# Kernel tuning notes

Measured on AMD Instinct MI355X. Metric: run time of the kernel, lower is better.

The kernel has to match this reference:

```python
import jax, jax.numpy as jnp
import numpy as np

B, S, D, H = 2, 2048, 1024, 16
HD = D // H  # head_dim = 64


def setup_inputs() -> dict:
    key = jax.random.key(0)
    ks = jax.random.split(key, 12)
    scale = 1.0 / np.sqrt(D)
    inp = {
        "query": jax.random.normal(ks[0], (B, S, D), jnp.float32),
        "key": jax.random.normal(ks[1], (B, S, D), jnp.float32),
        "value": jax.random.normal(ks[2], (B, S, D), jnp.float32),
        # causal mask, True = masked out; shape [B, q_len, k_len]
        "mask": jnp.broadcast_to(
            jnp.triu(jnp.ones((S, S), jnp.bool_), k=1), (B, S, S)
        ),
        "Wq": jax.random.normal(ks[3], (D, D), jnp.float32) * scale,
        "bq": jnp.zeros((D,), jnp.float32),
        "Wk": jax.random.normal(ks[4], (D, D), jnp.float32) * scale,
        "bk": jnp.zeros((D,), jnp.float32),
        "Wv": jax.random.normal(ks[5], (D, D), jnp.float32) * scale,
        "bv": jnp.zeros((D,), jnp.float32),
        "Wo": jax.random.normal(ks[6], (D, D), jnp.float32) * scale,
        "bo": jnp.zeros((D,), jnp.float32),
    }
    return inp


def _split_heads(x):
    b, s, _ = x.shape
    return x.reshape(b, s, H, HD).transpose(0, 2, 1, 3)  # [B,H,S,HD]


def reference(query, key, value, mask, Wq, bq, Wk, bk, Wv, bv, Wo, bo):
    # Linear layers use torch convention: y = x @ W.T + b, W is [out, in]
    q = _split_heads(query @ Wq.T + bq)
    k = _split_heads(key @ Wk.T + bk)
    v = _split_heads(value @ Wv.T + bv)
    scores = jnp.einsum("bhqd,bhkd->bhqk", q, k) / jnp.sqrt(jnp.float32(HD))
    # normalized mask [B,1,q,k]; True means masked
    scores = jnp.where(mask[:, None, :, :], jnp.finfo(scores.dtype).min, scores)
    attn = jax.nn.softmax(scores, axis=-1)  # dropout is identity in eval
    ctx = jnp.einsum("bhqk,bhkd->bhqd", attn, v)
    merged = ctx.transpose(0, 2, 1, 3).reshape(query.shape[0], -1, D)
    out = merged @ Wo.T + bo
    return out
```

## Files before the change

### kernel.cpp

```cpp
#include <hip/hip_runtime.h>

#define B_ 2
#define S_ 2048
#define D_ 1024
#define H_ 16
#define HD_ 64
#define M_ (B_ * S_)

typedef __bf16 bf16x8 __attribute__((ext_vector_type(8)));
typedef float f32x4 __attribute__((ext_vector_type(4)));

__device__ inline unsigned short f2bf(float f) {
    unsigned int u = __builtin_bit_cast(unsigned int, f);
    u += 0x7fffu + ((u >> 16) & 1u);
    return (unsigned short)(u >> 16);
}

__device__ inline unsigned int cvt_pk_bf16(float lo, float hi) {
    unsigned int r;
    asm("v_cvt_pk_bf16_f32 %0, %1, %2" : "=v"(r) : "v"(lo), "v"(hi));
    return r;
}

__device__ inline float fexp2(float x) { return __builtin_amdgcn_exp2f(x); }

__device__ inline void barrier_fence() {
    asm volatile("" ::: "memory");
    __builtin_amdgcn_s_barrier();
    asm volatile("" ::: "memory");
}

__device__ inline void async_ld16(const unsigned short* g, unsigned short* l) {
    __builtin_amdgcn_global_load_lds(
        (const __attribute__((address_space(1))) unsigned int*)g,
        (__attribute__((address_space(3))) unsigned int*)l, 16, 0, 0);
}

__global__ __launch_bounds__(256) void cvt_all(
    const float* __restrict__ i0, const float* __restrict__ i1, const float* __restrict__ i2,
    const float* __restrict__ i3, const float* __restrict__ i4, const float* __restrict__ i5,
    const float* __restrict__ i6,
    unsigned short* __restrict__ o0, unsigned short* __restrict__ o1, unsigned short* __restrict__ o2,
    unsigned short* __restrict__ o3, unsigned short* __restrict__ o4, unsigned short* __restrict__ o5,
    unsigned short* __restrict__ o6, int nbig, int nsmall) {
    int z = blockIdx.y;
    const float* in = (z == 0) ? i0 : (z == 1) ? i1 : (z == 2) ? i2 : (z == 3) ? i3
                     : (z == 4) ? i4 : (z == 5) ? i5 : i6;
    unsigned short* out = (z == 0) ? o0 : (z == 1) ? o1 : (z == 2) ? o2 : (z == 3) ? o3
                         : (z == 4) ? o4 : (z == 5) ? o5 : o6;
    int n = (z < 3) ? nbig : nsmall;
    int i = (blockIdx.x * 256 + threadIdx.x) * 4;
    if (i >= n) return;
    float4 v = *(const float4*)(in + i);
    ushort4 o;
    o.x = f2bf(v.x); o.y = f2bf(v.y); o.z = f2bf(v.z); o.w = f2bf(v.w);
    *(ushort4*)(out + i) = o;
}

__device__ inline void gemm_compute(const unsigned short* __restrict__ A,
                                    const unsigned short* __restrict__ W,
                                    int K, int m0, int n0,
                                    unsigned short* As0, unsigned short* As1,
                                    unsigned short* Bs0, unsigned short* Bs1,
                                    f32x4 acc[4][4]) {
    const int t = threadIdx.x;
    const int lane = t & 63, wave = t >> 6;
    const int ml = lane & 15, quad = lane >> 4;
    const int wr = (wave >> 1) * 64, wc = (wave & 1) * 64;
    const int srow = lane >> 2;
    const int schunk = (lane & 3) ^ ((lane >> 4) & 3);

    const f32x4 zero = {0.f, 0.f, 0.f, 0.f};
    for (int i = 0; i < 4; i++)
        for (int j = 0; j < 4; j++) acc[i][j] = zero;

    const int niter = K >> 5;

    auto issue = [&](int kt, unsigned short* As, unsigned short* Bs) {
        int k0 = kt << 5;
        for (int i = 0; i < 2; i++) {
            int r = wave * 32 + i * 16;
            async_ld16(A + (size_t)(m0 + r + srow) * K + k0 + schunk * 8, As + r * 32);
            async_ld16(W + (size_t)(n0 + r + srow) * K + k0 + schunk * 8, Bs + r * 32);
        }
    };

    issue(0, As0, Bs0);
    issue(1, As1, Bs1);
    asm volatile("s_waitcnt vmcnt(4)" ::: "memory");
    barrier_fence();

    for (int kt = 0; kt < niter; kt++) {
        unsigned short* As = (kt & 1) ? As1 : As0;
        unsigned short* Bs = (kt & 1) ? Bs1 : Bs0;

        bf16x8 af[4], bfr[4];
        for (int i = 0; i < 4; i++)
            af[i] = *(const bf16x8*)(As + (wr + i * 16 + ml) * 32 + ((quad ^ (ml >> 2)) << 3));
        for (int j = 0; j < 4; j++)
            bfr[j] = *(const bf16x8*)(Bs + (wc + j * 16 + ml) * 32 + ((quad ^ (ml >> 2)) << 3));
        for (int i = 0; i < 4; i++)
            for (int j = 0; j < 4; j++)
                acc[i][j] = __builtin_amdgcn_mfma_f32_16x16x32_bf16(af[i], bfr[j], acc[i][j], 0, 0, 0);

        barrier_fence();
        if (kt + 2 < niter) {
            issue(kt + 2, As, Bs);
            asm volatile("s_waitcnt vmcnt(4)" ::: "memory");
        } else {
            asm volatile("s_waitcnt vmcnt(0)" ::: "memory");
        }
        barrier_fence();
    }
}

__global__ __launch_bounds__(256) void gemm_qkv(
    const unsigned short* __restrict__ xq, const unsigned short* __restrict__ xk,
    const unsigned short* __restrict__ xv,
    const unsigned short* __restrict__ wq, const unsigned short* __restrict__ wk,
    const unsigned short* __restrict__ wv,
    const float* __restrict__ bq, const float* __restrict__ bk, const float* __restrict__ bv,
    unsigned short* __restrict__ oq, unsigned short* __restrict__ ok,
    unsigned short* __restrict__ ov) {
    extern __shared__ __align__(16) unsigned short smem[];
    unsigned short* As0 = smem;
    unsigned short* As1 = smem + 4096;
    unsigned short* Bs0 = smem + 8192;
    unsigned short* Bs1 = smem + 12288;

    int f = blockIdx.x + (blockIdx.y << 3) + (blockIdx.z << 8);
    int l = (f & 7) * 96 + (f >> 3);
    int bx = l & 7, by = (l >> 3) & 31, z = l >> 8;

    const unsigned short *A, *W;
    const float* bias;
    unsigned short* out;
    if (z == 0) { A = xq; W = wq; bias = bq; out = oq; }
    else if (z == 1) { A = xk; W = wk; bias = bk; out = ok; }
    else { A = xv; W = wv; bias = bv; out = ov; }

    int m0 = by * 128, n0 = bx * 128;
    f32x4 acc[4][4];
    gemm_compute(A, W, D_, m0, n0, As0, As1, Bs0, Bs1, acc);

    const int t = threadIdx.x, lane = t & 63, wave = t >> 6;
    const int ml = lane & 15, quad = lane >> 4;
    const int wr = (wave >> 1) * 64, wc = (wave & 1) * 64;

    unsigned short* Cs = smem;
    const float sc = (z == 0) ? 0.1803368801111204f : 1.0f;
    for (int i = 0; i < 4; i++)
        for (int j = 0; j < 4; j++) {
            int col = wc + j * 16 + ml;
            float bb = bias[n0 + col];
            for (int rg = 0; rg < 4; rg++) {
                int row = wr + i * 16 + quad * 4 + rg;
                unsigned short v = f2bf((acc[i][j][rg] + bb) * sc);
                if (z < 2) Cs[row * 136 + col] = v;
                else       Cs[col * 136 + row] = v;
            }
        }
    __syncthreads();

    const int r = t >> 1, hf = t & 1;
    if (z < 2) {
        unsigned short* dst = out + (size_t)(m0 + r) * D_ + n0 + hf * 64;
        const unsigned short* src = Cs + r * 136 + hf * 64;
        for (int i = 0; i < 8; i++)
            *(uint4*)(dst + i * 8) = *(const uint4*)(src + i * 8);
    } else {
        int n = n0 + r, h = n >> 6, d = n & 63;
        int b = m0 >> 11, s0 = m0 & 2047;
        unsigned short* dst = ov + ((size_t)((b * H_ + h) * 64 + d)) * S_ + s0 + hf * 64;
        const unsigned short* src = Cs + r * 136 + hf * 64;
        for (int i = 0; i < 8; i++)
            *(uint4*)(dst + i * 8) = *(const uint4*)(src + i * 8);
    }
}

__global__ __launch_bounds__(256) void gemm_out(const unsigned short* __restrict__ A,
                                                const unsigned short* __restrict__ W,
                                                const float* __restrict__ bias,
                                                float* __restrict__ out) {
    __shared__ unsigned short As0[128 * 32], As1[128 * 32], Bs0[128 * 32], Bs1[128 * 32];

    int f = blockIdx.x + (blockIdx.y << 3);
    int l = (f & 7) * 32 + (f >> 3);
    int bx = l & 7, by = l >> 3;

    int m0 = by * 128, n0 = bx * 128;
    f32x4 acc[4][4];
    gemm_compute(A, W, D_, m0, n0, As0, As1, Bs0, Bs1, acc);

    const int t = threadIdx.x, lane = t & 63, wave = t >> 6;
    const int ml = lane & 15, quad = lane >> 4;
    const int wr = (wave >> 1) * 64, wc = (wave & 1) * 64;
    for (int i = 0; i < 4; i++)
        for (int j = 0; j < 4; j++) {
            int n = n0 + wc + j * 16 + ml;
            float bb = bias[n];
            for (int rg = 0; rg < 4; rg++) {
                int m = m0 + wr + i * 16 + quad * 4 + rg;
                out[(size_t)m * D_ + n] = acc[i][j][rg] + bb;
            }
        }
}

__global__ __launch_bounds__(256) void attn_kernel(const unsigned short* __restrict__ qm,
                                                   const unsigned short* __restrict__ km,
                                                   const unsigned short* __restrict__ vt,
                                                   unsigned short* __restrict__ ctx) {
    __shared__ unsigned short Ks[128 * 64];
    __shared__ unsigned short Vs[64 * 128];

    const int g = blockIdx.x >> 5;
    const int qb = (g & 1) ? (g >> 1) : (31 - (g >> 1));
    const int bh = blockIdx.x & 31;
    const int b = bh >> 4, h = bh & 15;
    const size_t vbase = (size_t)bh * S_ * 64;
    const int t = threadIdx.x, lane = t & 63, wave = t >> 6;
    const int ml = lane & 15, quad = lane >> 4;
    const int lrow = lane >> 3;
    const int gchunk = (lane & 7) ^ lrow;
    const int vrow = lane >> 4;
    const int q0 = qb * 64;

    bf16x8 qf[2];
    {
        int qrow = q0 + wave * 16 + ml;
        const unsigned short* qp = qm + (size_t)(b * S_ + qrow) * D_ + h * 64;
        qf[0] = *(const bf16x8*)(qp + quad * 8);
        qf[1] = *(const bf16x8*)(qp + 32 + quad * 8);
    }

    const f32x4 zero = {0.f, 0.f, 0.f, 0.f};
    f32x4 acc[4];
    for (int j = 0; j < 4; j++) acc[j] = zero;
    float m_i = -INFINITY, l_i = 0.f;

    const int ntiles = (qb + 2) >> 1;

    auto issue_K = [&](int kt) {
        for (int i = 0; i < 4; i++) {
            int r = wave * 32 + i * 8;
            async_ld16(km + (size_t)(b * S_ + kt * 128 + r + lrow) * D_ + h * 64 + gchunk * 8,
                       Ks + r * 64);
        }
    };
    auto issue_V = [&](int kt) {
        for (int i = 0; i < 4; i++) {
            int dd = wave * 16 + i * 4;
            int d = dd + vrow;
            async_ld16(vt + vbase + (size_t)d * S_ + kt * 128 + (((lane & 15) ^ (d & 15)) << 3),
                       Vs + dd * 128);
        }
    };

    issue_K(0);
    issue_V(0);
    asm volatile("s_waitcnt vmcnt(0)" ::: "memory");
    barrier_fence();

    for (int kt = 0; kt < ntiles; kt++) {
        f32x4 sacc[8];
        for (int n = 0; n < 8; n++) sacc[n] = zero;
        __builtin_amdgcn_s_setprio(1);
        for (int n = 0; n < 8; n++)
            for (int kk = 0; kk < 2; kk++) {
                bf16x8 kf = *(const bf16x8*)(Ks + (n * 16 + ml) * 64 +
                                             (((kk * 4 + quad) ^ (ml & 7)) << 3));
                sacc[n] = __builtin_amdgcn_mfma_f32_16x16x32_bf16(kf, qf[kk], sacc[n], 0, 0, 0);
            }
        __builtin_amdgcn_s_setprio(0);

        const bool last = (kt == ntiles - 1);
        const int qidx = q0 + wave * 16 + ml;
        if (last) {
            for (int n = 0; n < 8; n++)
                for (int rg = 0; rg < 4; rg++) {
                    int kidx = kt * 128 + n * 16 + quad * 4 + rg;
                    if (kidx > qidx) sacc[n][rg] = -3.0e38f;
                }
        }

        float m01 = fmaxf(fmaxf(sacc[0][0], sacc[0][1]), fmaxf(sacc[0][2], sacc[0][3]));
        float m1 = fmaxf(fmaxf(sacc[1][0], sacc[1][1]), fmaxf(sacc[1][2], sacc[1][3]));
        float m2 = fmaxf(fmaxf(sacc[2][0], sacc[2][1]), fmaxf(sacc[2][2], sacc[2][3]));
        float m3 = fmaxf(fmaxf(sacc[3][0], sacc[3][1]), fmaxf(sacc[3][2], sacc[3][3]));
        float m4 = fmaxf(fmaxf(sacc[4][0], sacc[4][1]), fmaxf(sacc[4][2], sacc[4][3]));
        float m5 = fmaxf(fmaxf(sacc[5][0], sacc[5][1]), fmaxf(sacc[5][2], sacc[5][3]));
        float m6 = fmaxf(fmaxf(sacc[6][0], sacc[6][1]), fmaxf(sacc[6][2], sacc[6][3]));
        float m7 = fmaxf(fmaxf(sacc[7][0], sacc[7][1]), fmaxf(sacc[7][2], sacc[7][3]));
        float mx = fmaxf(fmaxf(fmaxf(m01, m1), fmaxf(m2, m3)),
                         fmaxf(fmaxf(m4, m5), fmaxf(m6, m7)));
        mx = fmaxf(mx, __shfl_xor(mx, 16));
        mx = fmaxf(mx, __shfl_xor(mx, 32));
        if (!__all(mx <= m_i + 8.0f)) {
            float mc = fmaxf(m_i, mx);
            float al = fexp2(m_i - mc);
            m_i = mc;
            float alT[4];
            for (int rg = 0; rg < 4; rg++) alT[rg] = __shfl(al, quad * 4 + rg);
            for (int j = 0; j < 4; j++)
                for (int rg = 0; rg < 4; rg++) acc[j][rg] *= alT[rg];
            l_i *= al;
        }
        for (int n = 0; n < 8; n++)
            for (int rg = 0; rg < 4; rg++) sacc[n][rg] = fexp2(sacc[n][rg] - m_i);
        float s0 = (sacc[0][0] + sacc[0][1]) + (sacc[0][2] + sacc[0][3]);
        float s1 = (sacc[1][0] + sacc[1][1]) + (sacc[1][2] + sacc[1][3]);
        float s2 = (sacc[2][0] + sacc[2][1]) + (sacc[2][2] + sacc[2][3]);
        float s3 = (sacc[3][0] + sacc[3][1]) + (sacc[3][2] + sacc[3][3]);
        float s4 = (sacc[4][0] + sacc[4][1]) + (sacc[4][2] + sacc[4][3]);
        float s5 = (sacc[5][0] + sacc[5][1]) + (sacc[5][2] + sacc[5][3]);
        float s6 = (sacc[6][0] + sacc[6][1]) + (sacc[6][2] + sacc[6][3]);
        float s7 = (sacc[7][0] + sacc[7][1]) + (sacc[7][2] + sacc[7][3]);
        float rs = ((s0 + s1) + (s2 + s3)) + ((s4 + s5) + (s6 + s7));
        rs += __shfl_xor(rs, 16);
        rs += __shfl_xor(rs, 32);
        l_i += rs;

        asm volatile("s_waitcnt vmcnt(0)" ::: "memory");
        barrier_fence();
        if (kt + 1 < ntiles) issue_K(kt + 1);

        __builtin_amdgcn_s_setprio(1);
        for (int n2 = 0; n2 < 4; n2++) {
            union { bf16x8 v; unsigned int w[4]; } pk;
            pk.w[0] = cvt_pk_bf16(sacc[2 * n2][0], sacc[2 * n2][1]);
            pk.w[1] = cvt_pk_bf16(sacc[2 * n2][2], sacc[2 * n2][3]);
            pk.w[2] = cvt_pk_bf16(sacc[2 * n2 + 1][0], sacc[2 * n2 + 1][1]);
            pk.w[3] = cvt_pk_bf16(sacc[2 * n2 + 1][2], sacc[2 * n2 + 1][3]);
            const int c0 = 4 * n2 + (quad >> 1);
            const int qo = (quad & 1) << 2;
            for (int j = 0; j < 4; j++) {
                int row = j * 16 + ml;
                union { bf16x8 v; uint2 d2[2]; } vv;
                vv.d2[0] = *(const uint2*)(Vs + row * 128 + (((c0 ^ (row & 15)) << 3) + qo));
                vv.d2[1] = *(const uint2*)(Vs + row * 128 + ((((c0 + 2) ^ (row & 15)) << 3) + qo));
                acc[j] = __builtin_amdgcn_mfma_f32_16x16x32_bf16(pk.v, vv.v, acc[j], 0, 0, 0);
            }
        }
        __builtin_amdgcn_s_setprio(0);

        if (kt + 1 < ntiles) {
            asm volatile("s_waitcnt vmcnt(0)" ::: "memory");
            barrier_fence();
            issue_V(kt + 1);
        }
    }

    float inv[4];
    for (int rg = 0; rg < 4; rg++) inv[rg] = __builtin_amdgcn_rcpf(__shfl(l_i, quad * 4 + rg));
    for (int j = 0; j < 4; j++) {
        int d = j * 16 + ml;
        for (int rg = 0; rg < 4; rg++) {
            int srow = q0 + wave * 16 + quad * 4 + rg;
            ctx[((size_t)(b * S_ + srow)) * D_ + h * 64 + d] = f2bf(acc[j][rg] * inv[rg]);
        }
    }
}

extern "C" void kernel_launch(void* const* d_in, const int* in_sizes, int n_in,
                              void* d_out, int out_size, void* d_ws, size_t ws_size,
                              hipStream_t stream) {
    const float* query = (const float*)d_in[0];
    const float* key_ = (const float*)d_in[1];
    const float* value = (const float*)d_in[2];
    const float* Wq = (const float*)d_in[4];
    const float* bq = (const float*)d_in[5];
    const float* Wk = (const float*)d_in[6];
    const float* bk = (const float*)d_in[7];
    const float* Wv = (const float*)d_in[8];
    const float* bv = (const float*)d_in[9];
    const float* Wo = (const float*)d_in[10];
    const float* bo = (const float*)d_in[11];
    float* out = (float*)d_out;

    const size_t XE = (size_t)M_ * D_;
    const size_t WE = (size_t)D_ * D_;
    char* ws = (char*)d_ws;
    unsigned short* xq = (unsigned short*)ws; ws += XE * 2;
    unsigned short* xk = (unsigned short*)ws; ws += XE * 2;
    unsigned short* xv = (unsigned short*)ws; ws += XE * 2;
    unsigned short* wqb = (unsigned short*)ws; ws += WE * 2;
    unsigned short* wkb = (unsigned short*)ws; ws += WE * 2;
    unsigned short* wvb = (unsigned short*)ws; ws += WE * 2;
    unsigned short* wob = (unsigned short*)ws; ws += WE * 2;
    unsigned short* qmb = (unsigned short*)ws; ws += XE * 2;
    unsigned short* kmb = (unsigned short*)ws; ws += XE * 2;
    unsigned short* vt = (unsigned short*)ws; ws += XE * 2;
    unsigned short* ctx = (unsigned short*)ws; ws += XE * 2;

    cvt_all<<<dim3(XE / 1024, 7), 256, 0, stream>>>(
        query, key_, value, Wq, Wk, Wv, Wo,
        xq, xk, xv, wqb, wkb, wvb, wob, (int)XE, (int)WE);

    gemm_qkv<<<dim3(D_ / 128, M_ / 128, 3), 256, 34816, stream>>>(
        xq, xk, xv, wqb, wkb, wvb, bq, bk, bv, qmb, kmb, vt);

    attn_kernel<<<dim3(1024), 256, 0, stream>>>(qmb, kmb, vt, ctx);

    gemm_out<<<dim3(D_ / 128, M_ / 128), 256, 0, stream>>>(ctx, wob, bo, out);
}
```

Baseline: 240.1 us.

## Double-buffer K/V tiles and pair complementary query blocks per attention workgroup

The attention kernel now keeps two LDS buffers for K and V and prefetches the next tile while computing the current one, with one barrier per tile instead of two. Each workgroup processes two query blocks (qb and 31-qb) so every block does the same causal work, and the grid is halved to 512. The row-max and row-sum cross-lane reductions are deferred: the max shuffle runs only on the rescale path and the sum shuffle once per query block. LDS use doubles, which may lower occupancy, and the grid is half as large.

```diff
diff --git a/kernel.cpp b/kernel.cpp
--- a/kernel.cpp
+++ b/kernel.cpp
@@ -210,11 +210,10 @@
                                                    const unsigned short* __restrict__ km,
                                                    const unsigned short* __restrict__ vt,
                                                    unsigned short* __restrict__ ctx) {
-    __shared__ unsigned short Ks[128 * 64];
-    __shared__ unsigned short Vs[64 * 128];
-
-    const int g = blockIdx.x >> 5;
-    const int qb = (g & 1) ? (g >> 1) : (31 - (g >> 1));
+    __shared__ unsigned short Ks[2][128 * 64];
+    __shared__ unsigned short Vs[2][64 * 128];
+
+    const int p = blockIdx.x >> 5;
     const int bh = blockIdx.x & 31;
     const int b = bh >> 4, h = bh & 15;
     const size_t vbase = (size_t)bh * S_ * 64;
@@ -223,140 +222,144 @@
     const int lrow = lane >> 3;
     const int gchunk = (lane & 7) ^ lrow;
     const int vrow = lane >> 4;
-    const int q0 = qb * 64;
-
-    bf16x8 qf[2];
-    {
-        int qrow = q0 + wave * 16 + ml;
-        const unsigned short* qp = qm + (size_t)(b * S_ + qrow) * D_ + h * 64;
-        qf[0] = *(const bf16x8*)(qp + quad * 8);
-        qf[1] = *(const bf16x8*)(qp + 32 + quad * 8);
-    }
-
-    const f32x4 zero = {0.f, 0.f, 0.f, 0.f};
-    f32x4 acc[4];
-    for (int j = 0; j < 4; j++) acc[j] = zero;
-    float m_i = -INFINITY, l_i = 0.f;
-
-    const int ntiles = (qb + 2) >> 1;
-
-    auto issue_K = [&](int kt) {
+
+    auto issue_K = [&](int kt, int bb) {
         for (int i = 0; i < 4; i++) {
             int r = wave * 32 + i * 8;
             async_ld16(km + (size_t)(b * S_ + kt * 128 + r + lrow) * D_ + h * 64 + gchunk * 8,
-                       Ks + r * 64);
+                       Ks[bb] + r * 64);
         }
     };
-    auto issue_V = [&](int kt) {
+    auto issue_V = [&](int kt, int bb) {
         for (int i = 0; i < 4; i++) {
             int dd = wave * 16 + i * 4;
             int d = dd + vrow;
             async_ld16(vt + vbase + (size_t)d * S_ + kt * 128 + (((lane & 15) ^ (d & 15)) << 3),
-                       Vs + dd * 128);
+                       Vs[bb] + dd * 128);
         }
     };
 
-    issue_K(0);
-    issue_V(0);
+    const f32x4 zero = {0.f, 0.f, 0.f, 0.f};
+
+    issue_K(0, 0);
+    issue_V(0, 0);
     asm volatile("s_waitcnt vmcnt(0)" ::: "memory");
     barrier_fence();
 
-    for (int kt = 0; kt < ntiles; kt++) {
-        f32x4 sacc[8];
-        for (int n = 0; n < 8; n++) sacc[n] = zero;
-        __builtin_amdgcn_s_setprio(1);
-        for (int n = 0; n < 8; n++)
-            for (int kk = 0; kk < 2; kk++) {
-                bf16x8 kf = *(const bf16x8*)(Ks + (n * 16 + ml) * 64 +
-                                             (((kk * 4 + quad) ^ (ml & 7)) << 3));
-                sacc[n] = __builtin_amdgcn_mfma_f32_16x16x32_bf16(kf, qf[kk], sacc[n], 0, 0, 0);
-            }
-        __builtin_amdgcn_s_setprio(0);
-
-        const bool last = (kt == ntiles - 1);
-        const int qidx = q0 + wave * 16 + ml;
-        if (last) {
+    int g = 0;
+    for (int s = 0; s < 2; s++) {
+        const int qb = s ? p : (31 - p);
+        const int q0 = qb * 64;
+        const int nt = (qb + 2) >> 1;
+
+        bf16x8 qf[2];
+        {
+            int qrow = q0 + wave * 16 + ml;
+            const unsigned short* qp = qm + (size_t)(b * S_ + qrow) * D_ + h * 64;
+            qf[0] = *(const bf16x8*)(qp + quad * 8);
+            qf[1] = *(const bf16x8*)(qp + 32 + quad * 8);
+        }
+
+        f32x4 acc[4];
+        for (int j = 0; j < 4; j++) acc[j] = zero;
+        float m_i = -INFINITY, lp = 0.f;
+
+        for (int kt = 0; kt < nt; kt++, g++) {
+            const int buf = g & 1;
+
+            if (kt + 1 < nt)  { issue_K(kt + 1, buf ^ 1); issue_V(kt + 1, buf ^ 1); }
+            else if (s == 0)  { issue_K(0, buf ^ 1);      issue_V(0, buf ^ 1); }
+
+            f32x4 sacc[8];
+            for (int n = 0; n < 8; n++) sacc[n] = zero;
+            __builtin_amdgcn_s_setprio(1);
             for (int n = 0; n < 8; n++)
-                for (int rg = 0; rg < 4; rg++) {
-                    int kidx = kt * 128 + n * 16 + quad * 4 + rg;
-                    if (kidx > qidx) sacc[n][rg] = -3.0e38f;
+                for (int kk = 0; kk < 2; kk++) {
+                    bf16x8 kf = *(const bf16x8*)(Ks[buf] + (n * 16 + ml) * 64 +
+                                                 (((kk * 4 + quad) ^ (ml & 7)) << 3));
+                    sacc[n] = __builtin_amdgcn_mfma_f32_16x16x32_bf16(kf, qf[kk], sacc[n], 0, 0, 0);
                 }
-        }
-
-        float m01 = fmaxf(fmaxf(sacc[0][0], sacc[0][1]), fmaxf(sacc[0][2], sacc[0][3]));
-        float m1 = fmaxf(fmaxf(sacc[1][0], sacc[1][1]), fmaxf(sacc[1][2], sacc[1][3]));
-        float m2 = fmaxf(fmaxf(sacc[2][0], sacc[2][1]), fmaxf(sacc[2][2], sacc[2][3]));
-        float m3 = fmaxf(fmaxf(sacc[3][0], sacc[3][1]), fmaxf(sacc[3][2], sacc[3][3]));
-        float m4 = fmaxf(fmaxf(sacc[4][0], sacc[4][1]), fmaxf(sacc[4][2], sacc[4][3]));
-        float m5 = fmaxf(fmaxf(sacc[5][0], sacc[5][1]), fmaxf(sacc[5][2], sacc[5][3]));
-        float m6 = fmaxf(fmaxf(sacc[6][0], sacc[6][1]), fmaxf(sacc[6][2], sacc[6][3]));
-        float m7 = fmaxf(fmaxf(sacc[7][0], sacc[7][1]), fmaxf(sacc[7][2], sacc[7][3]));
-        float mx = fmaxf(fmaxf(fmaxf(m01, m1), fmaxf(m2, m3)),
-                         fmaxf(fmaxf(m4, m5), fmaxf(m6, m7)));
-        mx = fmaxf(mx, __shfl_xor(mx, 16));
-        mx = fmaxf(mx, __shfl_xor(mx, 32));
-        if (!__all(mx <= m_i + 8.0f)) {
-            float mc = fmaxf(m_i, mx);
-            float al = fexp2(m_i - mc);
-            m_i = mc;
-            float alT[4];
-            for (int rg = 0; rg < 4; rg++) alT[rg] = __shfl(al, quad * 4 + rg);
-            for (int j = 0; j < 4; j++)
-                for (int rg = 0; rg < 4; rg++) acc[j][rg] *= alT[rg];
-            l_i *= al;
-        }
-        for (int n = 0; n < 8; n++)
-            for (int rg = 0; rg < 4; rg++) sacc[n][rg] = fexp2(sacc[n][rg] - m_i);
-        float s0 = (sacc[0][0] + sacc[0][1]) + (sacc[0][2] + sacc[0][3]);
-        float s1 = (sacc[1][0] + sacc[1][1]) + (sacc[1][2] + sacc[1][3]);
-        float s2 = (sacc[2][0] + sacc[2][1]) + (sacc[2][2] + sacc[2][3]);
-        float s3 = (sacc[3][0] + sacc[3][1]) + (sacc[3][2] + sacc[3][3]);
-        float s4 = (sacc[4][0] + sacc[4][1]) + (sacc[4][2] + sacc[4][3]);
-        float s5 = (sacc[5][0] + sacc[5][1]) + (sacc[5][2] + sacc[5][3]);
-        float s6 = (sacc[6][0] + sacc[6][1]) + (sacc[6][2] + sacc[6][3]);
-        float s7 = (sacc[7][0] + sacc[7][1]) + (sacc[7][2] + sacc[7][3]);
-        float rs = ((s0 + s1) + (s2 + s3)) + ((s4 + s5) + (s6 + s7));
-        rs += __shfl_xor(rs, 16);
-        rs += __shfl_xor(rs, 32);
-        l_i += rs;
-
-        asm volatile("s_waitcnt vmcnt(0)" ::: "memory");
-        barrier_fence();
-        if (kt + 1 < ntiles) issue_K(kt + 1);
-
-        __builtin_amdgcn_s_setprio(1);
-        for (int n2 = 0; n2 < 4; n2++) {
-            union { bf16x8 v; unsigned int w[4]; } pk;
-            pk.w[0] = cvt_pk_bf16(sacc[2 * n2][0], sacc[2 * n2][1]);
-            pk.w[1] = cvt_pk_bf16(sacc[2 * n2][2], sacc[2 * n2][3]);
-            pk.w[2] = cvt_pk_bf16(sacc[2 * n2 + 1][0], sacc[2 * n2 + 1][1]);
-            pk.w[3] = cvt_pk_bf16(sacc[2 * n2 + 1][2], sacc[2 * n2 + 1][3]);
-            const int c0 = 4 * n2 + (quad >> 1);
-            const int qo = (quad & 1) << 2;
-            for (int j = 0; j < 4; j++) {
-                int row = j * 16 + ml;
-                union { bf16x8 v; uint2 d2[2]; } vv;
-                vv.d2[0] = *(const uint2*)(Vs + row * 128 + (((c0 ^ (row & 15)) << 3) + qo));
-                vv.d2[1] = *(const uint2*)(Vs + row * 128 + ((((c0 + 2) ^ (row & 15)) << 3) + qo));
-                acc[j] = __builtin_amdgcn_mfma_f32_16x16x32_bf16(pk.v, vv.v, acc[j], 0, 0, 0);
-            }
-        }
-        __builtin_amdgcn_s_setprio(0);
-
-        if (kt + 1 < ntiles) {
+            __builtin_amdgcn_s_setprio(0);
+
+            const bool last = (kt == nt - 1);
+            const int qidx = q0 + wave * 16 + ml;
+            if (last) {
+                for (int n = 0; n < 8; n++)
+                    for (int rg = 0; rg < 4; rg++) {
+                        int kidx = kt * 128 + n * 16 + quad * 4 + rg;
+                        if (kidx > qidx) sacc[n][rg] = -3.0e38f;
+                    }
+            }
+
+            float m0v = fmaxf(fmaxf(sacc[0][0], sacc[0][1]), fmaxf(sacc[0][2], sacc[0][3]));
+            float m1 = fmaxf(fmaxf(sacc[1][0], sacc[1][1]), fmaxf(sacc[1][2], sacc[1][3]));
+            float m2 = fmaxf(fmaxf(sacc[2][0], sacc[2][1]), fmaxf(sacc[2][2], sacc[2][3]));
+            float m3 = fmaxf(fmaxf(sacc[3][0], sacc[3][1]), fmaxf(sacc[3][2], sacc[3][3]));
+            float m4 = fmaxf(fmaxf(sacc[4][0], sacc[4][1]), fmaxf(sacc[4][2], sacc[4][3]));
+            float m5 = fmaxf(fmaxf(sacc[5][0], sacc[5][1]), fmaxf(sacc[5][2], sacc[5][3]));
+            float m6 = fmaxf(fmaxf(sacc[6][0], sacc[6][1]), fmaxf(sacc[6][2], sacc[6][3]));
+            float m7 = fmaxf(fmaxf(sacc[7][0], sacc[7][1]), fmaxf(sacc[7][2], sacc[7][3]));
+            float mx = fmaxf(fmaxf(fmaxf(m0v, m1), fmaxf(m2, m3)),
+                             fmaxf(fmaxf(m4, m5), fmaxf(m6, m7)));
+
+            if (!__all(mx <= m_i + 8.0f)) {
+                float mc = fmaxf(mx, __shfl_xor(mx, 16));
+                mc = fmaxf(mc, __shfl_xor(mc, 32));
+                mc = fmaxf(m_i, mc);
+                float al = fexp2(m_i - mc);
+                m_i = mc;
+                float alT[4];
+                for (int rg = 0; rg < 4; rg++) alT[rg] = __shfl(al, quad * 4 + rg);
+                for (int j = 0; j < 4; j++)
+                    for (int rg = 0; rg < 4; rg++) acc[j][rg] *= alT[rg];
+                lp *= al;
+            }
+
+            for (int n = 0; n < 8; n++)
+                for (int rg = 0; rg < 4; rg++) sacc[n][rg] = fexp2(sacc[n][rg] - m_i);
+            float s0 = (sacc[0][0] + sacc[0][1]) + (sacc[0][2] + sacc[0][3]);
+            float s1 = (sacc[1][0] + sacc[1][1]) + (sacc[1][2] + sacc[1][3]);
+            float s2 = (sacc[2][0] + sacc[2][1]) + (sacc[2][2] + sacc[2][3]);
+            float s3 = (sacc[3][0] + sacc[3][1]) + (sacc[3][2] + sacc[3][3]);
+            float s4 = (sacc[4][0] + sacc[4][1]) + (sacc[4][2] + sacc[4][3]);
+            float s5 = (sacc[5][0] + sacc[5][1]) + (sacc[5][2] + sacc[5][3]);
+            float s6 = (sacc[6][0] + sacc[6][1]) + (sacc[6][2] + sacc[6][3]);
+            float s7 = (sacc[7][0] + sacc[7][1]) + (sacc[7][2] + sacc[7][3]);
+            lp += ((s0 + s1) + (s2 + s3)) + ((s4 + s5) + (s6 + s7));
+
+            __builtin_amdgcn_s_setprio(1);
+            for (int n2 = 0; n2 < 4; n2++) {
+                union { bf16x8 v; unsigned int w[4]; } pk;
+                pk.w[0] = cvt_pk_bf16(sacc[2 * n2][0], sacc[2 * n2][1]);
+                pk.w[1] = cvt_pk_bf16(sacc[2 * n2][2], sacc[2 * n2][3]);
+                pk.w[2] = cvt_pk_bf16(sacc[2 * n2 + 1][0], sacc[2 * n2 + 1][1]);
+                pk.w[3] = cvt_pk_bf16(sacc[2 * n2 + 1][2], sacc[2 * n2 + 1][3]);
+                const int c0 = 4 * n2 + (quad >> 1);
+                const int qo = (quad & 1) << 2;
+                for (int j = 0; j < 4; j++) {
+                    int row = j * 16 + ml;
+                    union { bf16x8 v; uint2 d2[2]; } vv;
+                    vv.d2[0] = *(const uint2*)(Vs[buf] + row * 128 + (((c0 ^ (row & 15)) << 3) + qo));
+                    vv.d2[1] = *(const uint2*)(Vs[buf] + row * 128 + ((((c0 + 2) ^ (row & 15)) << 3) + qo));
+                    acc[j] = __builtin_amdgcn_mfma_f32_16x16x32_bf16(pk.v, vv.v, acc[j], 0, 0, 0);
+                }
+            }
+            __builtin_amdgcn_s_setprio(0);
+
             asm volatile("s_waitcnt vmcnt(0)" ::: "memory");
             barrier_fence();
-            issue_V(kt + 1);
-        }
-    }
-
-    float inv[4];
-    for (int rg = 0; rg < 4; rg++) inv[rg] = __builtin_amdgcn_rcpf(__shfl(l_i, quad * 4 + rg));
-    for (int j = 0; j < 4; j++) {
-        int d = j * 16 + ml;
-        for (int rg = 0; rg < 4; rg++) {
-            int srow = q0 + wave * 16 + quad * 4 + rg;
-            ctx[((size_t)(b * S_ + srow)) * D_ + h * 64 + d] = f2bf(acc[j][rg] * inv[rg]);
+        }
+
+        float lc = lp + __shfl_xor(lp, 16);
+        lc += __shfl_xor(lc, 32);
+        float inv[4];
+        for (int rg = 0; rg < 4; rg++) inv[rg] = __builtin_amdgcn_rcpf(__shfl(lc, quad * 4 + rg));
+        for (int j = 0; j < 4; j++) {
+            int d = j * 16 + ml;
+            for (int rg = 0; rg < 4; rg++) {
+                int srow = q0 + wave * 16 + quad * 4 + rg;
+                ctx[((size_t)(b * S_ + srow)) * D_ + h * 64 + d] = f2bf(acc[j][rg] * inv[rg]);
+            }
         }
     }
 }
@@ -399,7 +402,7 @@
     gemm_qkv<<<dim3(D_ / 128, M_ / 128, 3), 256, 34816, stream>>>(
         xq, xk, xv, wqb, wkb, wvb, bq, bk, bv, qmb, kmb, vt);
 
-    attn_kernel<<<dim3(1024), 256, 0, stream>>>(qmb, kmb, vt, ctx);
+    attn_kernel<<<dim3(512), 256, 0, stream>>>(qmb, kmb, vt, ctx);
 
     gemm_out<<<dim3(D_ / 128, M_ / 128), 256, 0, stream>>>(ctx, wob, bo, out);
 }
```

Result: no change. 243.3 us (+1.4%).
